# Performance work log

Hardware: AMD Instinct MI355X
Metric: run time of the kernel (lower is better)

## Reference

```python
import jax, jax.numpy as jnp
import numpy as np


def setup_inputs() -> dict:
    key = jax.random.key(0)
    n_class, n_support, n_query, feature_dim = 32, 16, 16, 1024
    n_rows = n_class * n_support + n_query * n_class  # 1024
    data = jax.random.normal(key, (n_rows, feature_dim), dtype=jnp.float32)
    return {"data": data, "n_class": n_class, "n_support": n_support, "n_query": n_query}


def reference(data, n_class, n_support, n_query):
    D = data.shape[-1]
    # support: [n_class, n_support, D]; query: [n_query*n_class, D]
    support = data[: n_class * n_support].reshape(n_class, n_support, D)
    query = data[n_class * n_support :]
    # attention score: tanh(elementwise product) summed over feature dim
    # scores: [Q, n_class, n_support]  (Q = n_query*n_class)
    scores = jnp.tanh(support[None, :, :, :] * query[:, None, None, :]).sum(-1)
    att = jax.nn.softmax(scores, axis=-1)  # softmax over n_support
    # weighted instance pooling -> prototypes per (query, class): [Q, n_class, D]
    proto = jnp.einsum("qcs,csd->qcd", att, support)
    return proto
```

## Files before the change

### kernel.cpp

```cpp
#include <hip/hip_runtime.h>
#include <stdint.h>

constexpr int NC = 32, NS = 16, NQ = 512, D = 1024;
constexpr int QPB = 8;

typedef float v2f __attribute__((ext_vector_type(2)));
typedef float v4f __attribute__((ext_vector_type(4)));

__device__ __forceinline__ v2f quad_term(v2f t01, v2f t23) {
    v2f A, B;
    A.x = __builtin_amdgcn_exp2f(t01.x);
    A.y = __builtin_amdgcn_exp2f(t01.y);
    B.x = __builtin_amdgcn_exp2f(t23.x);
    B.y = __builtin_amdgcn_exp2f(t23.y);
    A += 1.f;
    B += 1.f;
    v2f prod = A * B;
    v2f sum  = A + B;
    v2f r;
    r.x = __builtin_amdgcn_rcpf(prod.x);
    r.y = __builtin_amdgcn_rcpf(prod.y);
    return sum * r;
}

__device__ __forceinline__ void gload_lds16(const float* g, float* l) {
    __builtin_amdgcn_global_load_lds(
        (const __attribute__((address_space(1))) void*)g,
        (__attribute__((address_space(3))) void*)l,
        16, 0, 0);
}

__global__ __launch_bounds__(256, 2)
void proto_attn_kernel(const float* __restrict__ data, float* __restrict__ out) {
    const int c    = blockIdx.x;
    const int qt   = blockIdx.y;
    const int tid  = threadIdx.x;
    const int wave = tid >> 6;
    const int lane = tid & 63;

    __shared__ __align__(16) float buf[2][NS * 256];

    const float* sup = data + (size_t)c * NS * D;
    const v4f*   sg4 = reinterpret_cast<const v4f*>(sup);

    auto stage = [&](int p, int b) {
        #pragma unroll
        for (int r = 0; r < 4; ++r) {
            int row = 4 * wave + r;
            gload_lds16(sup + row * D + p * 256 + lane * 4,
                        &buf[b][row * 256]);
        }
    };

    const float K = 2.88539008177792681472f;
    const int q0 = qt * QPB + wave * 2;
    const v4f* qg0 = reinterpret_cast<const v4f*>(data + (size_t)(NC * NS + q0) * D);
    const v4f* qg1 = qg0 + 256;

    stage(0, 0);
    __syncthreads();

    float sc0[NS], sc1[NS];
    #pragma unroll
    for (int s = 0; s < NS; ++s) { sc0[s] = 0.f; sc1[s] = 0.f; }

    #pragma unroll
    for (int p = 0; p < 4; ++p) {
        if (p < 3) stage(p + 1, (p + 1) & 1);
        v4f qA = qg0[(p << 6) + lane] * K;
        v4f qB = qg1[(p << 6) + lane] * K;
        const v4f* B = reinterpret_cast<const v4f*>(buf[p & 1]);
        #pragma unroll
        for (int s = 0; s < NS; ++s) {
            v4f sv = B[(s << 6) + lane];
            v2f t0 = quad_term(sv.xy * qA.xy, sv.zw * qA.zw);
            v2f t1 = quad_term(sv.xy * qB.xy, sv.zw * qB.zw);
            sc0[s] += t0.x + t0.y;
            sc1[s] += t1.x + t1.y;
        }
        if (p < 3) __syncthreads();
    }

    #pragma unroll
    for (int s = 0; s < NS; ++s) {
        float r0 = sc0[s], r1 = sc1[s];
        #pragma unroll
        for (int m = 32; m >= 1; m >>= 1) {
            r0 += __shfl_xor(r0, m, 64);
            r1 += __shfl_xor(r1, m, 64);
        }
        sc0[s] = (float)D - 2.f * r0;
        sc1[s] = (float)D - 2.f * r1;
    }

    const float L2E = 1.44269504088896340736f;
    float m0 = sc0[0], m1 = sc1[0];
    #pragma unroll
    for (int s = 1; s < NS; ++s) { m0 = fmaxf(m0, sc0[s]); m1 = fmaxf(m1, sc1[s]); }
    float sum0 = 0.f, sum1 = 0.f;
    #pragma unroll
    for (int s = 0; s < NS; ++s) {
        sc0[s] = __builtin_amdgcn_exp2f((sc0[s] - m0) * L2E);
        sc1[s] = __builtin_amdgcn_exp2f((sc1[s] - m1) * L2E);
        sum0 += sc0[s];
        sum1 += sc1[s];
    }
    const float inv0 = __builtin_amdgcn_rcpf(sum0);
    const float inv1 = __builtin_amdgcn_rcpf(sum1);
    #pragma unroll
    for (int s = 0; s < NS; ++s) { sc0[s] *= inv0; sc1[s] *= inv1; }

    v4f* og0 = reinterpret_cast<v4f*>(out + ((size_t)q0 * NC + c) * D);
    v4f* og1 = reinterpret_cast<v4f*>(out + ((size_t)(q0 + 1) * NC + c) * D);

    #pragma unroll
    for (int p = 0; p < 4; ++p) {
        v2f oxy0 = 0.f, ozw0 = 0.f, oxy1 = 0.f, ozw1 = 0.f;
        #pragma unroll
        for (int s = 0; s < NS; ++s) {
            v4f sv = sg4[(s << 8) + (p << 6) + lane];
            oxy0 += sv.xy * sc0[s];
            ozw0 += sv.zw * sc0[s];
            oxy1 += sv.xy * sc1[s];
            ozw1 += sv.zw * sc1[s];
        }
        v4f r0, r1;
        r0.xy = oxy0; r0.zw = ozw0;
        r1.xy = oxy1; r1.zw = ozw1;
        og0[(p << 6) + lane] = r0;
        og1[(p << 6) + lane] = r1;
    }
}

extern "C" void kernel_launch(void* const* d_in, const int* in_sizes, int n_in,
                              void* d_out, int out_size, void* d_ws, size_t ws_size,
                              hipStream_t stream) {
    (void)in_sizes; (void)n_in; (void)out_size; (void)d_ws; (void)ws_size;
    const float* data = (const float*)d_in[0];
    float* out = (float*)d_out;
    dim3 grid(NC, NQ / QPB);
    proto_attn_kernel<<<grid, dim3(256), 0, stream>>>(data, out);
}
```

Baseline: 134.9 us.

## Process four queries per wave and reuse LDS support tiles for pooling

Each wave now handles four queries instead of two, so the block covers 16 queries and each staged support tile in LDS serves twice as many queries. The pooling phase reads support from the LDS buffers that already hold quarters 2 and 3, then restages quarters 0 and 1, instead of reloading every support row from global memory. The tanh accumulation is folded into FMAs. The cost is more registers per thread (64 score accumulators), which may cause spills or lower occupancy, and half as many blocks in the grid.

```diff
diff --git a/kernel.cpp b/kernel.cpp
--- a/kernel.cpp
+++ b/kernel.cpp
@@ -2,12 +2,13 @@
 #include <stdint.h>
 
 constexpr int NC = 32, NS = 16, NQ = 512, D = 1024;
-constexpr int QPB = 8;
+constexpr int QPB = 16;
+constexpr int NQW = 4;
 
 typedef float v2f __attribute__((ext_vector_type(2)));
 typedef float v4f __attribute__((ext_vector_type(4)));
 
-__device__ __forceinline__ v2f quad_term(v2f t01, v2f t23) {
+__device__ __forceinline__ void quad_acc(v2f t01, v2f t23, float& acc) {
     v2f A, B;
     A.x = __builtin_amdgcn_exp2f(t01.x);
     A.y = __builtin_amdgcn_exp2f(t01.y);
@@ -17,10 +18,8 @@
     B += 1.f;
     v2f prod = A * B;
     v2f sum  = A + B;
-    v2f r;
-    r.x = __builtin_amdgcn_rcpf(prod.x);
-    r.y = __builtin_amdgcn_rcpf(prod.y);
-    return sum * r;
+    acc = fmaf(sum.x, __builtin_amdgcn_rcpf(prod.x), acc);
+    acc = fmaf(sum.y, __builtin_amdgcn_rcpf(prod.y), acc);
 }
 
 __device__ __forceinline__ void gload_lds16(const float* g, float* l) {
@@ -41,7 +40,6 @@
     __shared__ __align__(16) float buf[2][NS * 256];
 
     const float* sup = data + (size_t)c * NS * D;
-    const v4f*   sg4 = reinterpret_cast<const v4f*>(sup);
 
     auto stage = [&](int p, int b) {
         #pragma unroll
@@ -53,83 +51,93 @@
     };
 
     const float K = 2.88539008177792681472f;
-    const int q0 = qt * QPB + wave * 2;
-    const v4f* qg0 = reinterpret_cast<const v4f*>(data + (size_t)(NC * NS + q0) * D);
-    const v4f* qg1 = qg0 + 256;
+    const int q0 = qt * QPB + wave * NQW;
+    const v4f* qg = reinterpret_cast<const v4f*>(data + (size_t)(NC * NS + q0) * D);
 
     stage(0, 0);
     __syncthreads();
 
-    float sc0[NS], sc1[NS];
+    float sc[NQW][NS];
     #pragma unroll
-    for (int s = 0; s < NS; ++s) { sc0[s] = 0.f; sc1[s] = 0.f; }
+    for (int r = 0; r < NQW; ++r)
+        #pragma unroll
+        for (int s = 0; s < NS; ++s) sc[r][s] = 0.f;
 
     #pragma unroll
     for (int p = 0; p < 4; ++p) {
         if (p < 3) stage(p + 1, (p + 1) & 1);
-        v4f qA = qg0[(p << 6) + lane] * K;
-        v4f qB = qg1[(p << 6) + lane] * K;
+        v4f q[NQW];
+        #pragma unroll
+        for (int r = 0; r < NQW; ++r)
+            q[r] = qg[r * 256 + (p << 6) + lane] * K;
         const v4f* B = reinterpret_cast<const v4f*>(buf[p & 1]);
         #pragma unroll
         for (int s = 0; s < NS; ++s) {
             v4f sv = B[(s << 6) + lane];
-            v2f t0 = quad_term(sv.xy * qA.xy, sv.zw * qA.zw);
-            v2f t1 = quad_term(sv.xy * qB.xy, sv.zw * qB.zw);
-            sc0[s] += t0.x + t0.y;
-            sc1[s] += t1.x + t1.y;
+            #pragma unroll
+            for (int r = 0; r < NQW; ++r)
+                quad_acc(sv.xy * q[r].xy, sv.zw * q[r].zw, sc[r][s]);
         }
         if (p < 3) __syncthreads();
     }
 
     #pragma unroll
-    for (int s = 0; s < NS; ++s) {
-        float r0 = sc0[s], r1 = sc1[s];
+    for (int r = 0; r < NQW; ++r)
         #pragma unroll
-        for (int m = 32; m >= 1; m >>= 1) {
-            r0 += __shfl_xor(r0, m, 64);
-            r1 += __shfl_xor(r1, m, 64);
+        for (int s = 0; s < NS; ++s) {
+            float v = sc[r][s];
+            #pragma unroll
+            for (int m = 32; m >= 1; m >>= 1) v += __shfl_xor(v, m, 64);
+            sc[r][s] = (float)D - 2.f * v;
         }
-        sc0[s] = (float)D - 2.f * r0;
-        sc1[s] = (float)D - 2.f * r1;
+
+    const float L2E = 1.44269504088896340736f;
+    #pragma unroll
+    for (int r = 0; r < NQW; ++r) {
+        float mx = sc[r][0];
+        #pragma unroll
+        for (int s = 1; s < NS; ++s) mx = fmaxf(mx, sc[r][s]);
+        float sum = 0.f;
+        #pragma unroll
+        for (int s = 0; s < NS; ++s) {
+            sc[r][s] = __builtin_amdgcn_exp2f((sc[r][s] - mx) * L2E);
+            sum += sc[r][s];
+        }
+        const float inv = __builtin_amdgcn_rcpf(sum);
+        #pragma unroll
+        for (int s = 0; s < NS; ++s) sc[r][s] *= inv;
     }
 
-    const float L2E = 1.44269504088896340736f;
-    float m0 = sc0[0], m1 = sc1[0];
-    #pragma unroll
-    for (int s = 1; s < NS; ++s) { m0 = fmaxf(m0, sc0[s]); m1 = fmaxf(m1, sc1[s]); }
-    float sum0 = 0.f, sum1 = 0.f;
-    #pragma unroll
-    for (int s = 0; s < NS; ++s) {
-        sc0[s] = __builtin_amdgcn_exp2f((sc0[s] - m0) * L2E);
-        sc1[s] = __builtin_amdgcn_exp2f((sc1[s] - m1) * L2E);
-        sum0 += sc0[s];
-        sum1 += sc1[s];
-    }
-    const float inv0 = __builtin_amdgcn_rcpf(sum0);
-    const float inv1 = __builtin_amdgcn_rcpf(sum1);
-    #pragma unroll
-    for (int s = 0; s < NS; ++s) { sc0[s] *= inv0; sc1[s] *= inv1; }
-
-    v4f* og0 = reinterpret_cast<v4f*>(out + ((size_t)q0 * NC + c) * D);
-    v4f* og1 = reinterpret_cast<v4f*>(out + ((size_t)(q0 + 1) * NC + c) * D);
-
-    #pragma unroll
-    for (int p = 0; p < 4; ++p) {
-        v2f oxy0 = 0.f, ozw0 = 0.f, oxy1 = 0.f, ozw1 = 0.f;
+    auto proto_quarter = [&](int qq, int b) {
+        const v4f* B = reinterpret_cast<const v4f*>(buf[b]);
+        v2f oxy[NQW], ozw[NQW];
+        #pragma unroll
+        for (int r = 0; r < NQW; ++r) { oxy[r] = 0.f; ozw[r] = 0.f; }
         #pragma unroll
         for (int s = 0; s < NS; ++s) {
-            v4f sv = sg4[(s << 8) + (p << 6) + lane];
-            oxy0 += sv.xy * sc0[s];
-            ozw0 += sv.zw * sc0[s];
-            oxy1 += sv.xy * sc1[s];
-            ozw1 += sv.zw * sc1[s];
+            v4f sv = B[(s << 6) + lane];
+            #pragma unroll
+            for (int r = 0; r < NQW; ++r) {
+                oxy[r] += sv.xy * sc[r][s];
+                ozw[r] += sv.zw * sc[r][s];
+            }
         }
-        v4f r0, r1;
-        r0.xy = oxy0; r0.zw = ozw0;
-        r1.xy = oxy1; r1.zw = ozw1;
-        og0[(p << 6) + lane] = r0;
-        og1[(p << 6) + lane] = r1;
-    }
+        #pragma unroll
+        for (int r = 0; r < NQW; ++r) {
+            v4f o; o.xy = oxy[r]; o.zw = ozw[r];
+            v4f* og = reinterpret_cast<v4f*>(out + ((size_t)(q0 + r) * NC + c) * D);
+            og[(qq << 6) + lane] = o;
+        }
+    };
+
+    proto_quarter(2, 0);
+    proto_quarter(3, 1);
+    __syncthreads();
+    stage(0, 0);
+    stage(1, 1);
+    __syncthreads();
+    proto_quarter(0, 0);
+    proto_quarter(1, 1);
 }
 
 extern "C" void kernel_launch(void* const* d_in, const int* in_sizes, int n_in,
```

Result: slower. 141.7 us (+5.1%).
